# Optimization experiments

Measured on AMD Instinct MI355X. Metric: run time of the kernel, lower is better.

The kernel has to match this reference:

```python
import jax, jax.numpy as jnp
import numpy as np

C = 512
CQK = C // 8  # 64


def setup_inputs() -> dict:
    key = jax.random.key(0)
    ks = jax.random.split(key, 8)
    B, H, W = 16, 32, 32
    x = jax.random.normal(ks[0], (B, C, H, W), dtype=jnp.float32)
    # 1x1 conv weights stored as [out_ch, in_ch] matrices + biases
    sq = 1.0 / np.sqrt(C)
    Wq = jax.random.uniform(ks[1], (CQK, C), jnp.float32, -sq, sq)
    bq = jax.random.uniform(ks[2], (CQK,), jnp.float32, -sq, sq)
    Wk = jax.random.uniform(ks[3], (CQK, C), jnp.float32, -sq, sq)
    bk = jax.random.uniform(ks[4], (CQK,), jnp.float32, -sq, sq)
    Wv = jax.random.uniform(ks[5], (C, C), jnp.float32, -sq, sq)
    bv = jax.random.uniform(ks[6], (C,), jnp.float32, -sq, sq)
    gamma = jax.random.normal(ks[7], (1,), dtype=jnp.float32)
    return {"x": x, "Wq": Wq, "bq": bq, "Wk": Wk, "bk": bk, "Wv": Wv, "bv": bv, "gamma": gamma}


def reference(x, Wq, bq, Wk, bk, Wv, bv, gamma):
    B, Cin, H, W = x.shape
    xf = x.reshape(B, Cin, H * W)  # [B, C, N]
    # 1x1 convs == channel matmuls
    q = jnp.einsum('qc,bcn->bnq', Wq, xf) + bq[None, None, :]   # [B, N, Cqk]
    k = jnp.einsum('qc,bcn->bqn', Wk, xf) + bk[None, :, None]   # [B, Cqk, N]
    v = jnp.einsum('vc,bcn->bvn', Wv, xf) + bv[None, :, None]   # [B, C, N]
    scores = jnp.einsum('bnq,bqm->bnm', q, k)                    # [B, N, N]
    attn = jax.nn.softmax(scores, axis=-1)                       # softmax over keys
    # values @ attn^T : out[b,c,n] = sum_m v[b,c,m] * attn[b,n,m]
    attended = jnp.einsum('bvm,bnm->bvn', v, attn)               # [B, C, N]
    attended = attended.reshape(B, Cin, H, W)
    return gamma[0] * attended + x
```

## Files before the change

kernel.cpp:

```cpp
#include <hip/hip_runtime.h>
#include <stdint.h>

#define BB 16
#define CC 512
#define CQK 64
#define NN 1024

typedef __attribute__((ext_vector_type(8))) short bf16x8;
typedef __attribute__((ext_vector_type(4))) short short4v;
typedef __attribute__((ext_vector_type(8))) unsigned short ushort8;
typedef __attribute__((ext_vector_type(4))) float f32x4;

static __device__ __forceinline__ unsigned short f2bf(float f) {
  uint32_t u = __float_as_uint(f);
  u += 0x7FFFu + ((u >> 16) & 1u);
  return (unsigned short)(u >> 16);
}

static __device__ __forceinline__ void gll16(const unsigned short* g, unsigned short* l) {
  const __attribute__((address_space(1))) unsigned int* gp =
      reinterpret_cast<const __attribute__((address_space(1))) unsigned int*>(
          reinterpret_cast<uintptr_t>(g));
  __attribute__((address_space(3))) unsigned int* lp =
      reinterpret_cast<__attribute__((address_space(3))) unsigned int*>(
          (unsigned int)reinterpret_cast<uintptr_t>(l));
  __builtin_amdgcn_global_load_lds(gp, lp, 16, 0, 0);
}

__global__ __launch_bounds__(256) void k_pack_w(
    const float* __restrict__ Wq, const float* __restrict__ Wk,
    const float* __restrict__ Wv, unsigned short* __restrict__ Wall) {
  int idx = blockIdx.x * 256 + threadIdx.x;
  int e = idx * 4;
  if (e >= 640 * 512) return;
  int o = e >> 9;
  int c = e & 511;
  const float* src;
  if (o < 64)        src = Wq + (size_t)o * 512;
  else if (o < 128)  src = Wk + (size_t)(o - 64) * 512;
  else               src = Wv + (size_t)(o - 128) * 512;
  float4 v = *(const float4*)(src + c);
  short4v pk;
  pk[0] = (short)f2bf(v.x); pk[1] = (short)f2bf(v.y);
  pk[2] = (short)f2bf(v.z); pk[3] = (short)f2bf(v.w);
  *(short4v*)(Wall + e) = pk;
}

__global__ __launch_bounds__(256) void k_transpose_x(
    const float* __restrict__ x, unsigned short* __restrict__ xT) {
  __shared__ float tile[32][33];
  int b = blockIdx.z;
  int c0 = blockIdx.y * 32;
  int n0 = blockIdx.x * 32;
  int t = threadIdx.x;
  int tn = t & 31, tc = t >> 5;
  const float* xp = x + ((size_t)b * CC + c0) * NN + n0;
#pragma unroll
  for (int i = 0; i < 4; i++) {
    int c = tc + i * 8;
    tile[c][tn] = xp[(size_t)c * NN + tn];
  }
  __syncthreads();
  unsigned short* xq = xT + ((size_t)b * NN + n0) * CC + c0;
  int n = t >> 3;
  int cq = (t & 7) * 4;
  short4v pk;
#pragma unroll
  for (int k = 0; k < 4; k++) pk[k] = (short)f2bf(tile[cq + k][n]);
  *(short4v*)(&xq[(size_t)n * CC + cq]) = pk;
}

__global__ __launch_bounds__(256) void k_gemm1(
    const unsigned short* __restrict__ Wall, const unsigned short* __restrict__ xT,
    const float* __restrict__ bq, const float* __restrict__ bk,
    const float* __restrict__ bv,
    unsigned short* __restrict__ qkT, unsigned short* __restrict__ vbuf) {
  __shared__ __align__(16) unsigned short ldsA[2][128 * 32];
  __shared__ __align__(16) unsigned short ldsB[2][128 * 32];
  int bid = blockIdx.x;
  int swz = (bid & 7) * 80 + (bid >> 3);
  int nx = swz & 7;
  int rest = swz >> 3;
  int oy = rest % 5;
  int b = rest / 5;
  int o0 = oy * 128;
  int n0 = nx * 128;
  int t = threadIdx.x;
  int w = t >> 6, l = t & 63;
  int wm = w & 1, wn = w >> 1;
  int lr = l & 15, lq = l >> 4;

  f32x4 acc[4][4];
#pragma unroll
  for (int i = 0; i < 4; i++)
#pragma unroll
    for (int j = 0; j < 4; j++) acc[i][j] = (f32x4){0.f, 0.f, 0.f, 0.f};

  const unsigned short* Ab = Wall + (size_t)o0 * CC;
  const unsigned short* Bb = xT + ((size_t)b * NN + n0) * CC;
  int srow = t >> 2;
  int skq = (t & 3) * 8;
  int ldsw = (t >> 6) * 512;

#pragma unroll
  for (int p = 0; p < 2; p++) {
    int r = p * 64 + srow;
    gll16(&Ab[(size_t)r * CC + skq], &ldsA[0][p * 2048 + ldsw]);
    gll16(&Bb[(size_t)r * CC + skq], &ldsB[0][p * 2048 + ldsw]);
  }
  __syncthreads();

  for (int s = 0; s < 16; ++s) {
    int cur = s & 1;
    if (s + 1 < 16) {
      int kt = (s + 1) * 32;
#pragma unroll
      for (int p = 0; p < 2; p++) {
        int r = p * 64 + srow;
        gll16(&Ab[(size_t)r * CC + kt + skq], &ldsA[cur ^ 1][p * 2048 + ldsw]);
        gll16(&Bb[(size_t)r * CC + kt + skq], &ldsB[cur ^ 1][p * 2048 + ldsw]);
      }
    }
    bf16x8 af[4], bfr[4];
#pragma unroll
    for (int i = 0; i < 4; i++)
      af[i] = *(const bf16x8*)(&ldsA[cur][(wm * 64 + i * 16 + lr) * 32 + lq * 8]);
#pragma unroll
    for (int j = 0; j < 4; j++)
      bfr[j] = *(const bf16x8*)(&ldsB[cur][(wn * 64 + j * 16 + lr) * 32 + lq * 8]);
#pragma unroll
    for (int i = 0; i < 4; i++)
#pragma unroll
      for (int j = 0; j < 4; j++)
        acc[i][j] = __builtin_amdgcn_mfma_f32_16x16x32_bf16(af[i], bfr[j], acc[i][j], 0, 0, 0);
    __syncthreads();
  }

  if (o0 == 0) {
#pragma unroll
    for (int i = 0; i < 4; i++) {
      int ob = wm * 64 + i * 16 + lq * 4;
#pragma unroll
      for (int j = 0; j < 4; j++) {
        int n = n0 + wn * 64 + j * 16 + lr;
        short4v pk;
#pragma unroll
        for (int r = 0; r < 4; r++) {
          int o = ob + r;
          float bias = (o < 64) ? bq[o] : bk[o - 64];
          pk[r] = (short)f2bf(acc[i][j][r] + bias);
        }
        *(short4v*)(&qkT[((size_t)b * NN + n) * 128 + ob]) = pk;
      }
    }
  } else {
#pragma unroll
    for (int i = 0; i < 4; i++) {
#pragma unroll
      for (int r = 0; r < 4; r++) {
        int o = o0 + wm * 64 + i * 16 + lq * 4 + r;
        int c = o - 128;
        float bias = bv[c];
#pragma unroll
        for (int j = 0; j < 4; j++) {
          int n = n0 + wn * 64 + j * 16 + lr;
          vbuf[((size_t)b * CC + c) * NN + n] = f2bf(acc[i][j][r] + bias);
        }
      }
    }
  }
}

#define QT 64
#define MC 64
#define PSTR 72

__global__ __launch_bounds__(256, 2) void k_flash(
    const unsigned short* __restrict__ qkT, const unsigned short* __restrict__ vbuf,
    const float* __restrict__ x, const float* __restrict__ gamma,
    float* __restrict__ out) {
  __shared__ __align__(16) unsigned short P[QT * PSTR];
  __shared__ float red[4 * QT];
  __shared__ float fin[QT];

  int bid = blockIdx.x;
  int swz = (bid & 7) * 64 + (bid >> 3);
  int ntile = swz & 15;
  int chalf = (swz >> 4) & 1;
  int b = swz >> 5;
  int n0 = ntile * QT;
  int t = threadIdx.x;
  int w = t >> 6, l = t & 63;
  int lr = l & 15, lq = l >> 4;
  const unsigned short* qk = qkT + (size_t)b * NN * 128;
  const unsigned short* Vb = vbuf + ((size_t)b * CC + chalf * 256 + w * 64) * NN;

  bf16x8 aq[4][2];
#pragma unroll
  for (int nj = 0; nj < 4; nj++)
#pragma unroll
    for (int ks = 0; ks < 2; ks++)
      aq[nj][ks] = *(const bf16x8*)(&qk[(size_t)(n0 + nj * 16 + lr) * 128 + ks * 32 + lq * 8]);

  f32x4 acc[4][4];
#pragma unroll
  for (int ci = 0; ci < 4; ci++)
#pragma unroll
    for (int nj = 0; nj < 4; nj++) acc[ci][nj] = (f32x4){0.f, 0.f, 0.f, 0.f};
  float sreg[4][4];
#pragma unroll
  for (int nj = 0; nj < 4; nj++)
#pragma unroll
    for (int r = 0; r < 4; r++) sreg[nj][r] = 0.f;

  float ev[4][4];
  {
    int mrow = w * 16 + lr;
    bf16x8 kf0 = *(const bf16x8*)(&qk[(size_t)mrow * 128 + 64 + lq * 8]);
    bf16x8 kf1 = *(const bf16x8*)(&qk[(size_t)mrow * 128 + 96 + lq * 8]);
#pragma unroll
    for (int nj = 0; nj < 4; nj++) {
      f32x4 s = (f32x4){0.f, 0.f, 0.f, 0.f};
      s = __builtin_amdgcn_mfma_f32_16x16x32_bf16(aq[nj][0], kf0, s, 0, 0, 0);
      s = __builtin_amdgcn_mfma_f32_16x16x32_bf16(aq[nj][1], kf1, s, 0, 0, 0);
#pragma unroll
      for (int r = 0; r < 4; r++) {
        float e = __expf(s[r]);
        ev[nj][r] = e;
        sreg[nj][r] += e;
      }
    }
  }

  for (int m0 = 0; m0 < NN; m0 += MC) {
    bf16x8 af0[4];
#pragma unroll
    for (int ci = 0; ci < 4; ci++)
      af0[ci] = *(const bf16x8*)(&Vb[(size_t)(ci * 16 + lr) * NN + m0 + lq * 8]);

    bf16x8 kf0n, kf1n;
    if (m0 + MC < NN) {
      int mrow = m0 + MC + w * 16 + lr;
      kf0n = *(const bf16x8*)(&qk[(size_t)mrow * 128 + 64 + lq * 8]);
      kf1n = *(const bf16x8*)(&qk[(size_t)mrow * 128 + 96 + lq * 8]);
    }

    __syncthreads();
#pragma unroll
    for (int nj = 0; nj < 4; nj++)
#pragma unroll
      for (int r = 0; r < 4; r++)
        P[(nj * 16 + lq * 4 + r) * PSTR + w * 16 + lr] = f2bf(ev[nj][r]);

    if (m0 + MC < NN) {
#pragma unroll
      for (int nj = 0; nj < 4; nj++) {
        f32x4 s = (f32x4){0.f, 0.f, 0.f, 0.f};
        s = __builtin_amdgcn_mfma_f32_16x16x32_bf16(aq[nj][0], kf0n, s, 0, 0, 0);
        s = __builtin_amdgcn_mfma_f32_16x16x32_bf16(aq[nj][1], kf1n, s, 0, 0, 0);
#pragma unroll
        for (int r = 0; r < 4; r++) {
          float e = __expf(s[r]);
          ev[nj][r] = e;
          sreg[nj][r] += e;
        }
      }
    }
    __syncthreads();

    bf16x8 af1[4];
#pragma unroll
    for (int ci = 0; ci < 4; ci++)
      af1[ci] = *(const bf16x8*)(&Vb[(size_t)(ci * 16 + lr) * NN + m0 + 32 + lq * 8]);

#pragma unroll
    for (int nj = 0; nj < 4; nj++) {
      bf16x8 pf = *(const bf16x8*)(&P[(nj * 16 + lr) * PSTR + lq * 8]);
#pragma unroll
      for (int ci = 0; ci < 4; ci++)
        acc[ci][nj] = __builtin_amdgcn_mfma_f32_16x16x32_bf16(af0[ci], pf, acc[ci][nj], 0, 0, 0);
    }
#pragma unroll
    for (int nj = 0; nj < 4; nj++) {
      bf16x8 pf = *(const bf16x8*)(&P[(nj * 16 + lr) * PSTR + 32 + lq * 8]);
#pragma unroll
      for (int ci = 0; ci < 4; ci++)
        acc[ci][nj] = __builtin_amdgcn_mfma_f32_16x16x32_bf16(af1[ci], pf, acc[ci][nj], 0, 0, 0);
    }
  }

#pragma unroll
  for (int nj = 0; nj < 4; nj++)
#pragma unroll
    for (int r = 0; r < 4; r++) {
#pragma unroll
      for (int d = 1; d < 16; d <<= 1) sreg[nj][r] += __shfl_xor(sreg[nj][r], d, 64);
    }
  __syncthreads();
  if (lr == 0) {
#pragma unroll
    for (int nj = 0; nj < 4; nj++)
#pragma unroll
      for (int r = 0; r < 4; r++) red[w * QT + nj * 16 + lq * 4 + r] = sreg[nj][r];
  }
  __syncthreads();
  if (t < QT) {
    float ssum = red[t] + red[QT + t] + red[2 * QT + t] + red[3 * QT + t];
    fin[t] = ssum;
  }
  __syncthreads();

  float invL[4];
#pragma unroll
  for (int nj = 0; nj < 4; nj++) invL[nj] = 1.0f / fin[nj * 16 + lr];
  float g = gamma[0];
#pragma unroll
  for (int ci = 0; ci < 4; ci++) {
#pragma unroll
    for (int r = 0; r < 4; r++) {
      int c = chalf * 256 + w * 64 + ci * 16 + lq * 4 + r;
#pragma unroll
      for (int nj = 0; nj < 4; nj++) {
        size_t idx = ((size_t)b * CC + c) * NN + n0 + nj * 16 + lr;
        out[idx] = g * acc[ci][nj][r] * invL[nj] + x[idx];
      }
    }
  }
}

extern "C" void kernel_launch(void* const* d_in, const int* in_sizes, int n_in,
                              void* d_out, int out_size, void* d_ws, size_t ws_size,
                              hipStream_t stream) {
  (void)in_sizes; (void)n_in; (void)out_size; (void)ws_size;
  const float* x     = (const float*)d_in[0];
  const float* Wq    = (const float*)d_in[1];
  const float* bq    = (const float*)d_in[2];
  const float* Wk    = (const float*)d_in[3];
  const float* bk    = (const float*)d_in[4];
  const float* Wv    = (const float*)d_in[5];
  const float* bv    = (const float*)d_in[6];
  const float* gamma = (const float*)d_in[7];
  float* out = (float*)d_out;

  char* ws = (char*)d_ws;
  unsigned short* Wall = (unsigned short*)(ws);
  unsigned short* xT   = (unsigned short*)(ws + 655360);
  unsigned short* qkT  = (unsigned short*)(ws + 655360 + 16777216);
  unsigned short* vbuf = (unsigned short*)(ws + 655360 + 16777216 + 4194304);

  k_pack_w<<<dim3(320), dim3(256), 0, stream>>>(Wq, Wk, Wv, Wall);
  k_transpose_x<<<dim3(NN / 32, CC / 32, BB), dim3(256), 0, stream>>>(x, xT);
  k_gemm1<<<dim3(640), dim3(256), 0, stream>>>(Wall, xT, bq, bk, bv, qkT, vbuf);
  k_flash<<<dim3(512), dim3(256), 0, stream>>>(qkT, vbuf, x, gamma, out);
}
```

Baseline: 166.6 us.

## Fuse x transpose and bf16 conversion into projection GEMM operand loads

Removes the separate transpose/convert kernel and its 16 MB bf16 intermediate. The projection GEMM now reads fp32 x directly into registers in the MFMA B-operand layout, converting to bf16 on the fly with a one-stage register prefetch. The flash kernel also hoists the second V fragment load ahead of the barrier. In exchange, the global loads of x are scalar strided fp32 reads, each lane hitting 32 different rows. Each x tile is also re-read by five output-row blocks instead of once, and register pressure rises.

```diff
diff --git a/kernel.cpp b/kernel.cpp
--- a/kernel.cpp
+++ b/kernel.cpp
@@ -46,37 +46,12 @@
   *(short4v*)(Wall + e) = pk;
 }
 
-__global__ __launch_bounds__(256) void k_transpose_x(
-    const float* __restrict__ x, unsigned short* __restrict__ xT) {
-  __shared__ float tile[32][33];
-  int b = blockIdx.z;
-  int c0 = blockIdx.y * 32;
-  int n0 = blockIdx.x * 32;
-  int t = threadIdx.x;
-  int tn = t & 31, tc = t >> 5;
-  const float* xp = x + ((size_t)b * CC + c0) * NN + n0;
-#pragma unroll
-  for (int i = 0; i < 4; i++) {
-    int c = tc + i * 8;
-    tile[c][tn] = xp[(size_t)c * NN + tn];
-  }
-  __syncthreads();
-  unsigned short* xq = xT + ((size_t)b * NN + n0) * CC + c0;
-  int n = t >> 3;
-  int cq = (t & 7) * 4;
-  short4v pk;
-#pragma unroll
-  for (int k = 0; k < 4; k++) pk[k] = (short)f2bf(tile[cq + k][n]);
-  *(short4v*)(&xq[(size_t)n * CC + cq]) = pk;
-}
-
 __global__ __launch_bounds__(256) void k_gemm1(
-    const unsigned short* __restrict__ Wall, const unsigned short* __restrict__ xT,
+    const unsigned short* __restrict__ Wall, const float* __restrict__ x,
     const float* __restrict__ bq, const float* __restrict__ bk,
     const float* __restrict__ bv,
     unsigned short* __restrict__ qkT, unsigned short* __restrict__ vbuf) {
   __shared__ __align__(16) unsigned short ldsA[2][128 * 32];
-  __shared__ __align__(16) unsigned short ldsB[2][128 * 32];
   int bid = blockIdx.x;
   int swz = (bid & 7) * 80 + (bid >> 3);
   int nx = swz & 7;
@@ -97,7 +72,7 @@
     for (int j = 0; j < 4; j++) acc[i][j] = (f32x4){0.f, 0.f, 0.f, 0.f};
 
   const unsigned short* Ab = Wall + (size_t)o0 * CC;
-  const unsigned short* Bb = xT + ((size_t)b * NN + n0) * CC;
+  const float* xb2 = x + ((size_t)b * CC) * NN + n0 + wn * 64 + lr;
   int srow = t >> 2;
   int skq = (t & 3) * 8;
   int ldsw = (t >> 6) * 512;
@@ -106,33 +81,56 @@
   for (int p = 0; p < 2; p++) {
     int r = p * 64 + srow;
     gll16(&Ab[(size_t)r * CC + skq], &ldsA[0][p * 2048 + ldsw]);
-    gll16(&Bb[(size_t)r * CC + skq], &ldsB[0][p * 2048 + ldsw]);
+  }
+  float fB[4][8];
+#pragma unroll
+  for (int e = 0; e < 8; e++)
+#pragma unroll
+    for (int j = 0; j < 4; j++)
+      fB[j][e] = xb2[(size_t)(lq * 8 + e) * NN + j * 16];
+  bf16x8 bfr[4];
+#pragma unroll
+  for (int j = 0; j < 4; j++) {
+    bf16x8 v;
+#pragma unroll
+    for (int e = 0; e < 8; e++) v[e] = (short)f2bf(fB[j][e]);
+    bfr[j] = v;
   }
   __syncthreads();
 
   for (int s = 0; s < 16; ++s) {
     int cur = s & 1;
-    if (s + 1 < 16) {
+    if (s < 15) {
       int kt = (s + 1) * 32;
 #pragma unroll
       for (int p = 0; p < 2; p++) {
         int r = p * 64 + srow;
         gll16(&Ab[(size_t)r * CC + kt + skq], &ldsA[cur ^ 1][p * 2048 + ldsw]);
-        gll16(&Bb[(size_t)r * CC + kt + skq], &ldsB[cur ^ 1][p * 2048 + ldsw]);
-      }
-    }
-    bf16x8 af[4], bfr[4];
+      }
+#pragma unroll
+      for (int e = 0; e < 8; e++)
+#pragma unroll
+        for (int j = 0; j < 4; j++)
+          fB[j][e] = xb2[(size_t)(kt + lq * 8 + e) * NN + j * 16];
+    }
+    bf16x8 af[4];
 #pragma unroll
     for (int i = 0; i < 4; i++)
       af[i] = *(const bf16x8*)(&ldsA[cur][(wm * 64 + i * 16 + lr) * 32 + lq * 8]);
 #pragma unroll
-    for (int j = 0; j < 4; j++)
-      bfr[j] = *(const bf16x8*)(&ldsB[cur][(wn * 64 + j * 16 + lr) * 32 + lq * 8]);
-#pragma unroll
     for (int i = 0; i < 4; i++)
 #pragma unroll
       for (int j = 0; j < 4; j++)
         acc[i][j] = __builtin_amdgcn_mfma_f32_16x16x32_bf16(af[i], bfr[j], acc[i][j], 0, 0, 0);
+    if (s < 15) {
+#pragma unroll
+      for (int j = 0; j < 4; j++) {
+        bf16x8 v;
+#pragma unroll
+        for (int e = 0; e < 8; e++) v[e] = (short)f2bf(fB[j][e]);
+        bfr[j] = v;
+      }
+    }
     __syncthreads();
   }
 
@@ -233,10 +231,13 @@
   }
 
   for (int m0 = 0; m0 < NN; m0 += MC) {
-    bf16x8 af0[4];
+    bf16x8 af0[4], af1[4];
 #pragma unroll
     for (int ci = 0; ci < 4; ci++)
       af0[ci] = *(const bf16x8*)(&Vb[(size_t)(ci * 16 + lr) * NN + m0 + lq * 8]);
+#pragma unroll
+    for (int ci = 0; ci < 4; ci++)
+      af1[ci] = *(const bf16x8*)(&Vb[(size_t)(ci * 16 + lr) * NN + m0 + 32 + lq * 8]);
 
     bf16x8 kf0n, kf1n;
     if (m0 + MC < NN) {
@@ -267,11 +268,6 @@
       }
     }
     __syncthreads();
-
-    bf16x8 af1[4];
-#pragma unroll
-    for (int ci = 0; ci < 4; ci++)
-      af1[ci] = *(const bf16x8*)(&Vb[(size_t)(ci * 16 + lr) * NN + m0 + 32 + lq * 8]);
 
 #pragma unroll
     for (int nj = 0; nj < 4; nj++) {
@@ -344,12 +340,10 @@
 
   char* ws = (char*)d_ws;
   unsigned short* Wall = (unsigned short*)(ws);
-  unsigned short* xT   = (unsigned short*)(ws + 655360);
-  unsigned short* qkT  = (unsigned short*)(ws + 655360 + 16777216);
-  unsigned short* vbuf = (unsigned short*)(ws + 655360 + 16777216 + 4194304);
+  unsigned short* qkT  = (unsigned short*)(ws + 655360);
+  unsigned short* vbuf = (unsigned short*)(ws + 655360 + 4194304);
 
   k_pack_w<<<dim3(320), dim3(256), 0, stream>>>(Wq, Wk, Wv, Wall);
-  k_transpose_x<<<dim3(NN / 32, CC / 32, BB), dim3(256), 0, stream>>>(x, xT);
-  k_gemm1<<<dim3(640), dim3(256), 0, stream>>>(Wall, xT, bq, bk, bv, qkT, vbuf);
+  k_gemm1<<<dim3(640), dim3(256), 0, stream>>>(Wall, x, bq, bk, bv, qkT, vbuf);
   k_flash<<<dim3(512), dim3(256), 0, stream>>>(qkT, vbuf, x, gamma, out);
 }
```

After: 178.3 us. +7.0%, slower.

## Fuse all four kernels into one persistent kernel with grid barriers

Applied to the files above, without the earlier changes.

Replaces the four separate launches (weight pack, x transpose, projection GEMM, flash attention) with a single 640-block kernel whose phases are separated by a software grid barrier on a global atomic counter. The aim is to remove launch gaps and tail idle time between the kernels. It also raises launch bounds to 4 blocks per SM and hoists the second V fragment load earlier in the attention loop. The barrier assumes all 640 blocks are co-resident, has a spin timeout that could silently break ordering, and adds atomic spin overhead.

```diff
diff --git a/kernel.cpp b/kernel.cpp
--- a/kernel.cpp
+++ b/kernel.cpp
@@ -5,10 +5,10 @@
 #define CC 512
 #define CQK 64
 #define NN 1024
+#define NBLK 640
 
 typedef __attribute__((ext_vector_type(8))) short bf16x8;
 typedef __attribute__((ext_vector_type(4))) short short4v;
-typedef __attribute__((ext_vector_type(8))) unsigned short ushort8;
 typedef __attribute__((ext_vector_type(4))) float f32x4;
 
 static __device__ __forceinline__ unsigned short f2bf(float f) {
@@ -27,237 +27,226 @@
   __builtin_amdgcn_global_load_lds(gp, lp, 16, 0, 0);
 }
 
-__global__ __launch_bounds__(256) void k_pack_w(
-    const float* __restrict__ Wq, const float* __restrict__ Wk,
-    const float* __restrict__ Wv, unsigned short* __restrict__ Wall) {
-  int idx = blockIdx.x * 256 + threadIdx.x;
-  int e = idx * 4;
-  if (e >= 640 * 512) return;
-  int o = e >> 9;
-  int c = e & 511;
-  const float* src;
-  if (o < 64)        src = Wq + (size_t)o * 512;
-  else if (o < 128)  src = Wk + (size_t)(o - 64) * 512;
-  else               src = Wv + (size_t)(o - 128) * 512;
-  float4 v = *(const float4*)(src + c);
-  short4v pk;
-  pk[0] = (short)f2bf(v.x); pk[1] = (short)f2bf(v.y);
-  pk[2] = (short)f2bf(v.z); pk[3] = (short)f2bf(v.w);
-  *(short4v*)(Wall + e) = pk;
-}
-
-__global__ __launch_bounds__(256) void k_transpose_x(
-    const float* __restrict__ x, unsigned short* __restrict__ xT) {
-  __shared__ float tile[32][33];
-  int b = blockIdx.z;
-  int c0 = blockIdx.y * 32;
-  int n0 = blockIdx.x * 32;
-  int t = threadIdx.x;
-  int tn = t & 31, tc = t >> 5;
-  const float* xp = x + ((size_t)b * CC + c0) * NN + n0;
-#pragma unroll
-  for (int i = 0; i < 4; i++) {
-    int c = tc + i * 8;
-    tile[c][tn] = xp[(size_t)c * NN + tn];
-  }
+__device__ unsigned int g_bar = 0;
+
+static __device__ __forceinline__ void gridbar() {
   __syncthreads();
-  unsigned short* xq = xT + ((size_t)b * NN + n0) * CC + c0;
-  int n = t >> 3;
-  int cq = (t & 7) * 4;
-  short4v pk;
-#pragma unroll
-  for (int k = 0; k < 4; k++) pk[k] = (short)f2bf(tile[cq + k][n]);
-  *(short4v*)(&xq[(size_t)n * CC + cq]) = pk;
-}
-
-__global__ __launch_bounds__(256) void k_gemm1(
-    const unsigned short* __restrict__ Wall, const unsigned short* __restrict__ xT,
-    const float* __restrict__ bq, const float* __restrict__ bk,
-    const float* __restrict__ bv,
-    unsigned short* __restrict__ qkT, unsigned short* __restrict__ vbuf) {
-  __shared__ __align__(16) unsigned short ldsA[2][128 * 32];
-  __shared__ __align__(16) unsigned short ldsB[2][128 * 32];
-  int bid = blockIdx.x;
-  int swz = (bid & 7) * 80 + (bid >> 3);
-  int nx = swz & 7;
-  int rest = swz >> 3;
-  int oy = rest % 5;
-  int b = rest / 5;
-  int o0 = oy * 128;
-  int n0 = nx * 128;
-  int t = threadIdx.x;
-  int w = t >> 6, l = t & 63;
-  int wm = w & 1, wn = w >> 1;
-  int lr = l & 15, lq = l >> 4;
-
-  f32x4 acc[4][4];
-#pragma unroll
-  for (int i = 0; i < 4; i++)
-#pragma unroll
-    for (int j = 0; j < 4; j++) acc[i][j] = (f32x4){0.f, 0.f, 0.f, 0.f};
-
-  const unsigned short* Ab = Wall + (size_t)o0 * CC;
-  const unsigned short* Bb = xT + ((size_t)b * NN + n0) * CC;
-  int srow = t >> 2;
-  int skq = (t & 3) * 8;
-  int ldsw = (t >> 6) * 512;
-
-#pragma unroll
-  for (int p = 0; p < 2; p++) {
-    int r = p * 64 + srow;
-    gll16(&Ab[(size_t)r * CC + skq], &ldsA[0][p * 2048 + ldsw]);
-    gll16(&Bb[(size_t)r * CC + skq], &ldsB[0][p * 2048 + ldsw]);
+  __threadfence();
+  if (threadIdx.x == 0) {
+    unsigned int ticket =
+        __hip_atomic_fetch_add(&g_bar, 1u, __ATOMIC_RELAXED, __HIP_MEMORY_SCOPE_AGENT);
+    unsigned int target = (ticket / NBLK + 1u) * NBLK;
+    unsigned int spins = 0;
+    while (__hip_atomic_load(&g_bar, __ATOMIC_RELAXED, __HIP_MEMORY_SCOPE_AGENT) < target) {
+      __builtin_amdgcn_s_sleep(4);
+      if (++spins > (1u << 20)) break;
+    }
   }
   __syncthreads();
-
-  for (int s = 0; s < 16; ++s) {
-    int cur = s & 1;
-    if (s + 1 < 16) {
-      int kt = (s + 1) * 32;
-#pragma unroll
-      for (int p = 0; p < 2; p++) {
-        int r = p * 64 + srow;
-        gll16(&Ab[(size_t)r * CC + kt + skq], &ldsA[cur ^ 1][p * 2048 + ldsw]);
-        gll16(&Bb[(size_t)r * CC + kt + skq], &ldsB[cur ^ 1][p * 2048 + ldsw]);
-      }
-    }
-    bf16x8 af[4], bfr[4];
-#pragma unroll
-    for (int i = 0; i < 4; i++)
-      af[i] = *(const bf16x8*)(&ldsA[cur][(wm * 64 + i * 16 + lr) * 32 + lq * 8]);
-#pragma unroll
-    for (int j = 0; j < 4; j++)
-      bfr[j] = *(const bf16x8*)(&ldsB[cur][(wn * 64 + j * 16 + lr) * 32 + lq * 8]);
-#pragma unroll
-    for (int i = 0; i < 4; i++)
-#pragma unroll
-      for (int j = 0; j < 4; j++)
-        acc[i][j] = __builtin_amdgcn_mfma_f32_16x16x32_bf16(af[i], bfr[j], acc[i][j], 0, 0, 0);
-    __syncthreads();
-  }
-
-  if (o0 == 0) {
-#pragma unroll
-    for (int i = 0; i < 4; i++) {
-      int ob = wm * 64 + i * 16 + lq * 4;
-#pragma unroll
-      for (int j = 0; j < 4; j++) {
-        int n = n0 + wn * 64 + j * 16 + lr;
-        short4v pk;
-#pragma unroll
-        for (int r = 0; r < 4; r++) {
-          int o = ob + r;
-          float bias = (o < 64) ? bq[o] : bk[o - 64];
-          pk[r] = (short)f2bf(acc[i][j][r] + bias);
-        }
-        *(short4v*)(&qkT[((size_t)b * NN + n) * 128 + ob]) = pk;
-      }
-    }
-  } else {
-#pragma unroll
-    for (int i = 0; i < 4; i++) {
-#pragma unroll
-      for (int r = 0; r < 4; r++) {
-        int o = o0 + wm * 64 + i * 16 + lq * 4 + r;
-        int c = o - 128;
-        float bias = bv[c];
-#pragma unroll
-        for (int j = 0; j < 4; j++) {
-          int n = n0 + wn * 64 + j * 16 + lr;
-          vbuf[((size_t)b * CC + c) * NN + n] = f2bf(acc[i][j][r] + bias);
-        }
-      }
-    }
-  }
+  __threadfence();
 }
 
 #define QT 64
 #define MC 64
 #define PSTR 72
 
-__global__ __launch_bounds__(256, 2) void k_flash(
-    const unsigned short* __restrict__ qkT, const unsigned short* __restrict__ vbuf,
-    const float* __restrict__ x, const float* __restrict__ gamma,
+__global__ __launch_bounds__(256, 4) void k_fused(
+    const float* __restrict__ x,
+    const float* __restrict__ Wq, const float* __restrict__ bq,
+    const float* __restrict__ Wk, const float* __restrict__ bk,
+    const float* __restrict__ Wv, const float* __restrict__ bv,
+    const float* __restrict__ gamma,
+    unsigned short* __restrict__ Wall, unsigned short* __restrict__ xT,
+    unsigned short* __restrict__ qkT, unsigned short* __restrict__ vbuf,
     float* __restrict__ out) {
-  __shared__ __align__(16) unsigned short P[QT * PSTR];
-  __shared__ float red[4 * QT];
-  __shared__ float fin[QT];
+  __shared__ __align__(16) char lds_raw[32768];
 
   int bid = blockIdx.x;
-  int swz = (bid & 7) * 64 + (bid >> 3);
-  int ntile = swz & 15;
-  int chalf = (swz >> 4) & 1;
-  int b = swz >> 5;
-  int n0 = ntile * QT;
   int t = threadIdx.x;
-  int w = t >> 6, l = t & 63;
-  int lr = l & 15, lq = l >> 4;
-  const unsigned short* qk = qkT + (size_t)b * NN * 128;
-  const unsigned short* Vb = vbuf + ((size_t)b * CC + chalf * 256 + w * 64) * NN;
-
-  bf16x8 aq[4][2];
-#pragma unroll
-  for (int nj = 0; nj < 4; nj++)
-#pragma unroll
-    for (int ks = 0; ks < 2; ks++)
-      aq[nj][ks] = *(const bf16x8*)(&qk[(size_t)(n0 + nj * 16 + lr) * 128 + ks * 32 + lq * 8]);
-
-  f32x4 acc[4][4];
-#pragma unroll
-  for (int ci = 0; ci < 4; ci++)
-#pragma unroll
-    for (int nj = 0; nj < 4; nj++) acc[ci][nj] = (f32x4){0.f, 0.f, 0.f, 0.f};
-  float sreg[4][4];
-#pragma unroll
-  for (int nj = 0; nj < 4; nj++)
-#pragma unroll
-    for (int r = 0; r < 4; r++) sreg[nj][r] = 0.f;
-
-  float ev[4][4];
+
+  if (bid < 320) {
+    int e = (bid * 256 + t) * 4;
+    int o = e >> 9;
+    int c = e & 511;
+    const float* src;
+    if (o < 64)        src = Wq + (size_t)o * 512;
+    else if (o < 128)  src = Wk + (size_t)(o - 64) * 512;
+    else               src = Wv + (size_t)(o - 128) * 512;
+    float4 v = *(const float4*)(src + c);
+    short4v pk;
+    pk[0] = (short)f2bf(v.x); pk[1] = (short)f2bf(v.y);
+    pk[2] = (short)f2bf(v.z); pk[3] = (short)f2bf(v.w);
+    *(short4v*)(Wall + e) = pk;
+  }
+
   {
-    int mrow = w * 16 + lr;
-    bf16x8 kf0 = *(const bf16x8*)(&qk[(size_t)mrow * 128 + 64 + lq * 8]);
-    bf16x8 kf1 = *(const bf16x8*)(&qk[(size_t)mrow * 128 + 96 + lq * 8]);
-#pragma unroll
-    for (int nj = 0; nj < 4; nj++) {
-      f32x4 s = (f32x4){0.f, 0.f, 0.f, 0.f};
-      s = __builtin_amdgcn_mfma_f32_16x16x32_bf16(aq[nj][0], kf0, s, 0, 0, 0);
-      s = __builtin_amdgcn_mfma_f32_16x16x32_bf16(aq[nj][1], kf1, s, 0, 0, 0);
-#pragma unroll
-      for (int r = 0; r < 4; r++) {
-        float e = __expf(s[r]);
-        ev[nj][r] = e;
-        sreg[nj][r] += e;
-      }
-    }
-  }
-
-  for (int m0 = 0; m0 < NN; m0 += MC) {
-    bf16x8 af0[4];
+    float (*tile)[33] = (float (*)[33])lds_raw;
+    int tn = t & 31, tc = t >> 5;
+    for (int tau = bid; tau < 8192; tau += NBLK) {
+      int bz = tau >> 9;
+      int by = (tau >> 5) & 15;
+      int bx = tau & 31;
+      int c0 = by * 32, n0 = bx * 32;
+      const float* xp = x + ((size_t)bz * CC + c0) * NN + n0;
+#pragma unroll
+      for (int i = 0; i < 4; i++) {
+        int c = tc + i * 8;
+        tile[c][tn] = xp[(size_t)c * NN + tn];
+      }
+      __syncthreads();
+      unsigned short* xq = xT + ((size_t)bz * NN + n0) * CC + c0;
+      int n = t >> 3;
+      int cq = (t & 7) * 4;
+      short4v pk;
+#pragma unroll
+      for (int k = 0; k < 4; k++) pk[k] = (short)f2bf(tile[cq + k][n]);
+      *(short4v*)(&xq[(size_t)n * CC + cq]) = pk;
+      __syncthreads();
+    }
+  }
+
+  gridbar();
+
+  {
+    unsigned short* ldsA = (unsigned short*)lds_raw;
+    unsigned short* ldsB = ldsA + 8192;
+    int swz = (bid & 7) * 80 + (bid >> 3);
+    int nx = swz & 7;
+    int rest = swz >> 3;
+    int oy = rest % 5;
+    int b = rest / 5;
+    int o0 = oy * 128;
+    int n0 = nx * 128;
+    int w = t >> 6, l = t & 63;
+    int wm = w & 1, wn = w >> 1;
+    int lr = l & 15, lq = l >> 4;
+
+    f32x4 acc[4][4];
+#pragma unroll
+    for (int i = 0; i < 4; i++)
+#pragma unroll
+      for (int j = 0; j < 4; j++) acc[i][j] = (f32x4){0.f, 0.f, 0.f, 0.f};
+
+    const unsigned short* Ab = Wall + (size_t)o0 * CC;
+    const unsigned short* Bb = xT + ((size_t)b * NN + n0) * CC;
+    int srow = t >> 2;
+    int skq = (t & 3) * 8;
+    int ldsw = (t >> 6) * 512;
+
+#pragma unroll
+    for (int p = 0; p < 2; p++) {
+      int r = p * 64 + srow;
+      gll16(&Ab[(size_t)r * CC + skq], &ldsA[p * 2048 + ldsw]);
+      gll16(&Bb[(size_t)r * CC + skq], &ldsB[p * 2048 + ldsw]);
+    }
+    __syncthreads();
+
+    for (int s = 0; s < 16; ++s) {
+      int cur = s & 1;
+      if (s + 1 < 16) {
+        int kt = (s + 1) * 32;
+#pragma unroll
+        for (int p = 0; p < 2; p++) {
+          int r = p * 64 + srow;
+          gll16(&Ab[(size_t)r * CC + kt + skq], &ldsA[(cur ^ 1) * 4096 + p * 2048 + ldsw]);
+          gll16(&Bb[(size_t)r * CC + kt + skq], &ldsB[(cur ^ 1) * 4096 + p * 2048 + ldsw]);
+        }
+      }
+      bf16x8 af[4], bfr[4];
+#pragma unroll
+      for (int i = 0; i < 4; i++)
+        af[i] = *(const bf16x8*)(&ldsA[cur * 4096 + (wm * 64 + i * 16 + lr) * 32 + lq * 8]);
+#pragma unroll
+      for (int j = 0; j < 4; j++)
+        bfr[j] = *(const bf16x8*)(&ldsB[cur * 4096 + (wn * 64 + j * 16 + lr) * 32 + lq * 8]);
+#pragma unroll
+      for (int i = 0; i < 4; i++)
+#pragma unroll
+        for (int j = 0; j < 4; j++)
+          acc[i][j] = __builtin_amdgcn_mfma_f32_16x16x32_bf16(af[i], bfr[j], acc[i][j], 0, 0, 0);
+      __syncthreads();
+    }
+
+    if (o0 == 0) {
+#pragma unroll
+      for (int i = 0; i < 4; i++) {
+        int ob = wm * 64 + i * 16 + lq * 4;
+#pragma unroll
+        for (int j = 0; j < 4; j++) {
+          int n = n0 + wn * 64 + j * 16 + lr;
+          short4v pk;
+#pragma unroll
+          for (int r = 0; r < 4; r++) {
+            int o = ob + r;
+            float bias = (o < 64) ? bq[o] : bk[o - 64];
+            pk[r] = (short)f2bf(acc[i][j][r] + bias);
+          }
+          *(short4v*)(&qkT[((size_t)b * NN + n) * 128 + ob]) = pk;
+        }
+      }
+    } else {
+#pragma unroll
+      for (int i = 0; i < 4; i++) {
+#pragma unroll
+        for (int r = 0; r < 4; r++) {
+          int o = o0 + wm * 64 + i * 16 + lq * 4 + r;
+          int c = o - 128;
+          float bias = bv[c];
+#pragma unroll
+          for (int j = 0; j < 4; j++) {
+            int n = n0 + wn * 64 + j * 16 + lr;
+            vbuf[((size_t)b * CC + c) * NN + n] = f2bf(acc[i][j][r] + bias);
+          }
+        }
+      }
+    }
+  }
+
+  gridbar();
+
+  if (bid < 512) {
+    unsigned short* P = (unsigned short*)lds_raw;
+    float* red = (float*)(lds_raw + 9216);
+    float* fin = (float*)(lds_raw + 9216 + 1024);
+
+    int swz = (bid & 7) * 64 + (bid >> 3);
+    int ntile = swz & 15;
+    int chalf = (swz >> 4) & 1;
+    int b = swz >> 5;
+    int n0 = ntile * QT;
+    int w = t >> 6, l = t & 63;
+    int lr = l & 15, lq = l >> 4;
+    const unsigned short* qk = qkT + (size_t)b * NN * 128;
+    const unsigned short* Vb = vbuf + ((size_t)b * CC + chalf * 256 + w * 64) * NN;
+
+    bf16x8 aq[4][2];
+#pragma unroll
+    for (int nj = 0; nj < 4; nj++)
+#pragma unroll
+      for (int ks = 0; ks < 2; ks++)
+        aq[nj][ks] = *(const bf16x8*)(&qk[(size_t)(n0 + nj * 16 + lr) * 128 + ks * 32 + lq * 8]);
+
+    f32x4 acc[4][4];
 #pragma unroll
     for (int ci = 0; ci < 4; ci++)
-      af0[ci] = *(const bf16x8*)(&Vb[(size_t)(ci * 16 + lr) * NN + m0 + lq * 8]);
-
-    bf16x8 kf0n, kf1n;
-    if (m0 + MC < NN) {
-      int mrow = m0 + MC + w * 16 + lr;
-      kf0n = *(const bf16x8*)(&qk[(size_t)mrow * 128 + 64 + lq * 8]);
-      kf1n = *(const bf16x8*)(&qk[(size_t)mrow * 128 + 96 + lq * 8]);
-    }
-
-    __syncthreads();
+#pragma unroll
+      for (int nj = 0; nj < 4; nj++) acc[ci][nj] = (f32x4){0.f, 0.f, 0.f, 0.f};
+    float sreg[4][4];
 #pragma unroll
     for (int nj = 0; nj < 4; nj++)
 #pragma unroll
-      for (int r = 0; r < 4; r++)
-        P[(nj * 16 + lq * 4 + r) * PSTR + w * 16 + lr] = f2bf(ev[nj][r]);
-
-    if (m0 + MC < NN) {
+      for (int r = 0; r < 4; r++) sreg[nj][r] = 0.f;
+
+    float ev[4][4];
+    {
+      int mrow = w * 16 + lr;
+      bf16x8 kf0 = *(const bf16x8*)(&qk[(size_t)mrow * 128 + 64 + lq * 8]);
+      bf16x8 kf1 = *(const bf16x8*)(&qk[(size_t)mrow * 128 + 96 + lq * 8]);
 #pragma unroll
       for (int nj = 0; nj < 4; nj++) {
         f32x4 s = (f32x4){0.f, 0.f, 0.f, 0.f};
-        s = __builtin_amdgcn_mfma_f32_16x16x32_bf16(aq[nj][0], kf0n, s, 0, 0, 0);
-        s = __builtin_amdgcn_mfma_f32_16x16x32_bf16(aq[nj][1], kf1n, s, 0, 0, 0);
+        s = __builtin_amdgcn_mfma_f32_16x16x32_bf16(aq[nj][0], kf0, s, 0, 0, 0);
+        s = __builtin_amdgcn_mfma_f32_16x16x32_bf16(aq[nj][1], kf1, s, 0, 0, 0);
 #pragma unroll
         for (int r = 0; r < 4; r++) {
           float e = __expf(s[r]);
@@ -266,63 +255,97 @@
         }
       }
     }
+
+    for (int m0 = 0; m0 < NN; m0 += MC) {
+      bf16x8 af0[4], af1[4];
+#pragma unroll
+      for (int ci = 0; ci < 4; ci++)
+        af0[ci] = *(const bf16x8*)(&Vb[(size_t)(ci * 16 + lr) * NN + m0 + lq * 8]);
+#pragma unroll
+      for (int ci = 0; ci < 4; ci++)
+        af1[ci] = *(const bf16x8*)(&Vb[(size_t)(ci * 16 + lr) * NN + m0 + 32 + lq * 8]);
+
+      bf16x8 kf0n, kf1n;
+      if (m0 + MC < NN) {
+        int mrow = m0 + MC + w * 16 + lr;
+        kf0n = *(const bf16x8*)(&qk[(size_t)mrow * 128 + 64 + lq * 8]);
+        kf1n = *(const bf16x8*)(&qk[(size_t)mrow * 128 + 96 + lq * 8]);
+      }
+
+      __syncthreads();
+#pragma unroll
+      for (int nj = 0; nj < 4; nj++)
+#pragma unroll
+        for (int r = 0; r < 4; r++)
+          P[(nj * 16 + lq * 4 + r) * PSTR + w * 16 + lr] = f2bf(ev[nj][r]);
+
+      if (m0 + MC < NN) {
+#pragma unroll
+        for (int nj = 0; nj < 4; nj++) {
+          f32x4 s = (f32x4){0.f, 0.f, 0.f, 0.f};
+          s = __builtin_amdgcn_mfma_f32_16x16x32_bf16(aq[nj][0], kf0n, s, 0, 0, 0);
+          s = __builtin_amdgcn_mfma_f32_16x16x32_bf16(aq[nj][1], kf1n, s, 0, 0, 0);
+#pragma unroll
+          for (int r = 0; r < 4; r++) {
+            float e = __expf(s[r]);
+            ev[nj][r] = e;
+            sreg[nj][r] += e;
+          }
+        }
+      }
+      __syncthreads();
+
+#pragma unroll
+      for (int nj = 0; nj < 4; nj++) {
+        bf16x8 pf = *(const bf16x8*)(&P[(nj * 16 + lr) * PSTR + lq * 8]);
+#pragma unroll
+        for (int ci = 0; ci < 4; ci++)
+          acc[ci][nj] = __builtin_amdgcn_mfma_f32_16x16x32_bf16(af0[ci], pf, acc[ci][nj], 0, 0, 0);
+      }
+#pragma unroll
+      for (int nj = 0; nj < 4; nj++) {
+        bf16x8 pf = *(const bf16x8*)(&P[(nj * 16 + lr) * PSTR + 32 + lq * 8]);
+#pragma unroll
+        for (int ci = 0; ci < 4; ci++)
+          acc[ci][nj] = __builtin_amdgcn_mfma_f32_16x16x32_bf16(af1[ci], pf, acc[ci][nj], 0, 0, 0);
+      }
+    }
+
+#pragma unroll
+    for (int nj = 0; nj < 4; nj++)
+#pragma unroll
+      for (int r = 0; r < 4; r++) {
+#pragma unroll
+        for (int d = 1; d < 16; d <<= 1) sreg[nj][r] += __shfl_xor(sreg[nj][r], d, 64);
+      }
     __syncthreads();
-
-    bf16x8 af1[4];
-#pragma unroll
-    for (int ci = 0; ci < 4; ci++)
-      af1[ci] = *(const bf16x8*)(&Vb[(size_t)(ci * 16 + lr) * NN + m0 + 32 + lq * 8]);
-
-#pragma unroll
-    for (int nj = 0; nj < 4; nj++) {
-      bf16x8 pf = *(const bf16x8*)(&P[(nj * 16 + lr) * PSTR + lq * 8]);
-#pragma unroll
-      for (int ci = 0; ci < 4; ci++)
-        acc[ci][nj] = __builtin_amdgcn_mfma_f32_16x16x32_bf16(af0[ci], pf, acc[ci][nj], 0, 0, 0);
-    }
-#pragma unroll
-    for (int nj = 0; nj < 4; nj++) {
-      bf16x8 pf = *(const bf16x8*)(&P[(nj * 16 + lr) * PSTR + 32 + lq * 8]);
-#pragma unroll
-      for (int ci = 0; ci < 4; ci++)
-        acc[ci][nj] = __builtin_amdgcn_mfma_f32_16x16x32_bf16(af1[ci], pf, acc[ci][nj], 0, 0, 0);
-    }
-  }
-
-#pragma unroll
-  for (int nj = 0; nj < 4; nj++)
-#pragma unroll
-    for (int r = 0; r < 4; r++) {
-#pragma unroll
-      for (int d = 1; d < 16; d <<= 1) sreg[nj][r] += __shfl_xor(sreg[nj][r], d, 64);
-    }
-  __syncthreads();
-  if (lr == 0) {
-#pragma unroll
-    for (int nj = 0; nj < 4; nj++)
-#pragma unroll
-      for (int r = 0; r < 4; r++) red[w * QT + nj * 16 + lq * 4 + r] = sreg[nj][r];
-  }
-  __syncthreads();
-  if (t < QT) {
-    float ssum = red[t] + red[QT + t] + red[2 * QT + t] + red[3 * QT + t];
-    fin[t] = ssum;
-  }
-  __syncthreads();
-
-  float invL[4];
-#pragma unroll
-  for (int nj = 0; nj < 4; nj++) invL[nj] = 1.0f / fin[nj * 16 + lr];
-  float g = gamma[0];
-#pragma unroll
-  for (int ci = 0; ci < 4; ci++) {
-#pragma unroll
-    for (int r = 0; r < 4; r++) {
-      int c = chalf * 256 + w * 64 + ci * 16 + lq * 4 + r;
-#pragma unroll
-      for (int nj = 0; nj < 4; nj++) {
-        size_t idx = ((size_t)b * CC + c) * NN + n0 + nj * 16 + lr;
-        out[idx] = g * acc[ci][nj][r] * invL[nj] + x[idx];
+    if (lr == 0) {
+#pragma unroll
+      for (int nj = 0; nj < 4; nj++)
+#pragma unroll
+        for (int r = 0; r < 4; r++) red[w * QT + nj * 16 + lq * 4 + r] = sreg[nj][r];
+    }
+    __syncthreads();
+    if (t < QT) {
+      float ssum = red[t] + red[QT + t] + red[2 * QT + t] + red[3 * QT + t];
+      fin[t] = ssum;
+    }
+    __syncthreads();
+
+    float invL[4];
+#pragma unroll
+    for (int nj = 0; nj < 4; nj++) invL[nj] = 1.0f / fin[nj * 16 + lr];
+    float g = gamma[0];
+#pragma unroll
+    for (int ci = 0; ci < 4; ci++) {
+#pragma unroll
+      for (int r = 0; r < 4; r++) {
+        int c = chalf * 256 + w * 64 + ci * 16 + lq * 4 + r;
+#pragma unroll
+        for (int nj = 0; nj < 4; nj++) {
+          size_t idx = ((size_t)b * CC + c) * NN + n0 + nj * 16 + lr;
+          out[idx] = g * acc[ci][nj][r] * invL[nj] + x[idx];
+        }
       }
     }
   }
@@ -348,8 +371,6 @@
   unsigned short* qkT  = (unsigned short*)(ws + 655360 + 16777216);
   unsigned short* vbuf = (unsigned short*)(ws + 655360 + 16777216 + 4194304);
 
-  k_pack_w<<<dim3(320), dim3(256), 0, stream>>>(Wq, Wk, Wv, Wall);
-  k_transpose_x<<<dim3(NN / 32, CC / 32, BB), dim3(256), 0, stream>>>(x, xT);
-  k_gemm1<<<dim3(640), dim3(256), 0, stream>>>(Wall, xT, bq, bk, bv, qkT, vbuf);
-  k_flash<<<dim3(512), dim3(256), 0, stream>>>(qkT, vbuf, x, gamma, out);
-}
+  k_fused<<<dim3(NBLK), dim3(256), 0, stream>>>(
+      x, Wq, bq, Wk, bk, Wv, bv, gamma, Wall, xT, qkT, vbuf, out);
+}
```

Result: slower. 541.2 us (+224.8%).

## Fuse weight packing into transpose kernel and deepen V/K prefetch in flash loop

Applied to the files above, without the earlier changes.

Folds the weight bf16 packing into the x-transpose kernel, so the first 320 blocks also convert weights and one launch is removed. In the attention kernel, V fragments for the next chunk and K fragments two chunks ahead are prefetched into registers, so global-load latency is overlapped across loop iterations instead of stalling inside each one. The cost is higher register pressure, which under launch_bounds(256,2) may cause spills or lower occupancy.

```diff
diff --git a/kernel.cpp b/kernel.cpp
--- a/kernel.cpp
+++ b/kernel.cpp
@@ -8,7 +8,6 @@
 
 typedef __attribute__((ext_vector_type(8))) short bf16x8;
 typedef __attribute__((ext_vector_type(4))) short short4v;
-typedef __attribute__((ext_vector_type(8))) unsigned short ushort8;
 typedef __attribute__((ext_vector_type(4))) float f32x4;
 
 static __device__ __forceinline__ unsigned short f2bf(float f) {
@@ -27,32 +26,32 @@
   __builtin_amdgcn_global_load_lds(gp, lp, 16, 0, 0);
 }
 
-__global__ __launch_bounds__(256) void k_pack_w(
+__global__ __launch_bounds__(256) void k_prep(
+    const float* __restrict__ x, unsigned short* __restrict__ xT,
     const float* __restrict__ Wq, const float* __restrict__ Wk,
     const float* __restrict__ Wv, unsigned short* __restrict__ Wall) {
-  int idx = blockIdx.x * 256 + threadIdx.x;
-  int e = idx * 4;
-  if (e >= 640 * 512) return;
-  int o = e >> 9;
-  int c = e & 511;
-  const float* src;
-  if (o < 64)        src = Wq + (size_t)o * 512;
-  else if (o < 128)  src = Wk + (size_t)(o - 64) * 512;
-  else               src = Wv + (size_t)(o - 128) * 512;
-  float4 v = *(const float4*)(src + c);
-  short4v pk;
-  pk[0] = (short)f2bf(v.x); pk[1] = (short)f2bf(v.y);
-  pk[2] = (short)f2bf(v.z); pk[3] = (short)f2bf(v.w);
-  *(short4v*)(Wall + e) = pk;
-}
-
-__global__ __launch_bounds__(256) void k_transpose_x(
-    const float* __restrict__ x, unsigned short* __restrict__ xT) {
   __shared__ float tile[32][33];
   int b = blockIdx.z;
   int c0 = blockIdx.y * 32;
   int n0 = blockIdx.x * 32;
   int t = threadIdx.x;
+
+  int flat = ((int)blockIdx.z * gridDim.y + blockIdx.y) * gridDim.x + blockIdx.x;
+  if (flat < 320) {
+    int e = (flat * 256 + t) * 4;
+    int o = e >> 9;
+    int c = e & 511;
+    const float* src;
+    if (o < 64)        src = Wq + (size_t)o * 512;
+    else if (o < 128)  src = Wk + (size_t)(o - 64) * 512;
+    else               src = Wv + (size_t)(o - 128) * 512;
+    float4 v = *(const float4*)(src + c);
+    short4v pk;
+    pk[0] = (short)f2bf(v.x); pk[1] = (short)f2bf(v.y);
+    pk[2] = (short)f2bf(v.z); pk[3] = (short)f2bf(v.w);
+    *(short4v*)(Wall + e) = pk;
+  }
+
   int tn = t & 31, tc = t >> 5;
   const float* xp = x + ((size_t)b * CC + c0) * NN + n0;
 #pragma unroll
@@ -192,6 +191,7 @@
   int t = threadIdx.x;
   int w = t >> 6, l = t & 63;
   int lr = l & 15, lq = l >> 4;
+  int lq8 = lq * 8;
   const unsigned short* qk = qkT + (size_t)b * NN * 128;
   const unsigned short* Vb = vbuf + ((size_t)b * CC + chalf * 256 + w * 64) * NN;
 
@@ -200,7 +200,7 @@
   for (int nj = 0; nj < 4; nj++)
 #pragma unroll
     for (int ks = 0; ks < 2; ks++)
-      aq[nj][ks] = *(const bf16x8*)(&qk[(size_t)(n0 + nj * 16 + lr) * 128 + ks * 32 + lq * 8]);
+      aq[nj][ks] = *(const bf16x8*)(&qk[(size_t)(n0 + nj * 16 + lr) * 128 + ks * 32 + lq8]);
 
   f32x4 acc[4][4];
 #pragma unroll
@@ -213,11 +213,21 @@
 #pragma unroll
     for (int r = 0; r < 4; r++) sreg[nj][r] = 0.f;
 
+  bf16x8 vA[4];
+#pragma unroll
+  for (int ci = 0; ci < 4; ci++)
+    vA[ci] = *(const bf16x8*)(&Vb[(size_t)(ci * 16 + lr) * NN + lq8]);
+  bf16x8 kf0c, kf1c;
+  {
+    int mrow = MC + w * 16 + lr;
+    kf0c = *(const bf16x8*)(&qk[(size_t)mrow * 128 + 64 + lq8]);
+    kf1c = *(const bf16x8*)(&qk[(size_t)mrow * 128 + 96 + lq8]);
+  }
   float ev[4][4];
   {
     int mrow = w * 16 + lr;
-    bf16x8 kf0 = *(const bf16x8*)(&qk[(size_t)mrow * 128 + 64 + lq * 8]);
-    bf16x8 kf1 = *(const bf16x8*)(&qk[(size_t)mrow * 128 + 96 + lq * 8]);
+    bf16x8 kf0 = *(const bf16x8*)(&qk[(size_t)mrow * 128 + 64 + lq8]);
+    bf16x8 kf1 = *(const bf16x8*)(&qk[(size_t)mrow * 128 + 96 + lq8]);
 #pragma unroll
     for (int nj = 0; nj < 4; nj++) {
       f32x4 s = (f32x4){0.f, 0.f, 0.f, 0.f};
@@ -233,16 +243,22 @@
   }
 
   for (int m0 = 0; m0 < NN; m0 += MC) {
-    bf16x8 af0[4];
+    bool hn = (m0 + MC < NN);
+    bf16x8 vB[4];
 #pragma unroll
     for (int ci = 0; ci < 4; ci++)
-      af0[ci] = *(const bf16x8*)(&Vb[(size_t)(ci * 16 + lr) * NN + m0 + lq * 8]);
-
+      vB[ci] = *(const bf16x8*)(&Vb[(size_t)(ci * 16 + lr) * NN + m0 + 32 + lq8]);
+    bf16x8 vAn[4];
+    if (hn) {
+#pragma unroll
+      for (int ci = 0; ci < 4; ci++)
+        vAn[ci] = *(const bf16x8*)(&Vb[(size_t)(ci * 16 + lr) * NN + m0 + MC + lq8]);
+    }
     bf16x8 kf0n, kf1n;
-    if (m0 + MC < NN) {
-      int mrow = m0 + MC + w * 16 + lr;
-      kf0n = *(const bf16x8*)(&qk[(size_t)mrow * 128 + 64 + lq * 8]);
-      kf1n = *(const bf16x8*)(&qk[(size_t)mrow * 128 + 96 + lq * 8]);
+    if (m0 + 2 * MC < NN) {
+      int mrow = m0 + 2 * MC + w * 16 + lr;
+      kf0n = *(const bf16x8*)(&qk[(size_t)mrow * 128 + 64 + lq8]);
+      kf1n = *(const bf16x8*)(&qk[(size_t)mrow * 128 + 96 + lq8]);
     }
 
     __syncthreads();
@@ -252,12 +268,12 @@
       for (int r = 0; r < 4; r++)
         P[(nj * 16 + lq * 4 + r) * PSTR + w * 16 + lr] = f2bf(ev[nj][r]);
 
-    if (m0 + MC < NN) {
+    if (hn) {
 #pragma unroll
       for (int nj = 0; nj < 4; nj++) {
         f32x4 s = (f32x4){0.f, 0.f, 0.f, 0.f};
-        s = __builtin_amdgcn_mfma_f32_16x16x32_bf16(aq[nj][0], kf0n, s, 0, 0, 0);
-        s = __builtin_amdgcn_mfma_f32_16x16x32_bf16(aq[nj][1], kf1n, s, 0, 0, 0);
+        s = __builtin_amdgcn_mfma_f32_16x16x32_bf16(aq[nj][0], kf0c, s, 0, 0, 0);
+        s = __builtin_amdgcn_mfma_f32_16x16x32_bf16(aq[nj][1], kf1c, s, 0, 0, 0);
 #pragma unroll
         for (int r = 0; r < 4; r++) {
           float e = __expf(s[r]);
@@ -268,24 +284,26 @@
     }
     __syncthreads();
 
-    bf16x8 af1[4];
-#pragma unroll
-    for (int ci = 0; ci < 4; ci++)
-      af1[ci] = *(const bf16x8*)(&Vb[(size_t)(ci * 16 + lr) * NN + m0 + 32 + lq * 8]);
-
 #pragma unroll
     for (int nj = 0; nj < 4; nj++) {
-      bf16x8 pf = *(const bf16x8*)(&P[(nj * 16 + lr) * PSTR + lq * 8]);
+      bf16x8 pf = *(const bf16x8*)(&P[(nj * 16 + lr) * PSTR + lq8]);
 #pragma unroll
       for (int ci = 0; ci < 4; ci++)
-        acc[ci][nj] = __builtin_amdgcn_mfma_f32_16x16x32_bf16(af0[ci], pf, acc[ci][nj], 0, 0, 0);
+        acc[ci][nj] = __builtin_amdgcn_mfma_f32_16x16x32_bf16(vA[ci], pf, acc[ci][nj], 0, 0, 0);
     }
 #pragma unroll
     for (int nj = 0; nj < 4; nj++) {
-      bf16x8 pf = *(const bf16x8*)(&P[(nj * 16 + lr) * PSTR + 32 + lq * 8]);
+      bf16x8 pf = *(const bf16x8*)(&P[(nj * 16 + lr) * PSTR + 32 + lq8]);
 #pragma unroll
       for (int ci = 0; ci < 4; ci++)
-        acc[ci][nj] = __builtin_amdgcn_mfma_f32_16x16x32_bf16(af1[ci], pf, acc[ci][nj], 0, 0, 0);
+        acc[ci][nj] = __builtin_amdgcn_mfma_f32_16x16x32_bf16(vB[ci], pf, acc[ci][nj], 0, 0, 0);
+    }
+
+    if (hn) {
+#pragma unroll
+      for (int ci = 0; ci < 4; ci++) vA[ci] = vAn[ci];
+      kf0c = kf0n;
+      kf1c = kf1n;
     }
   }
 
@@ -348,8 +366,7 @@
   unsigned short* qkT  = (unsigned short*)(ws + 655360 + 16777216);
   unsigned short* vbuf = (unsigned short*)(ws + 655360 + 16777216 + 4194304);
 
-  k_pack_w<<<dim3(320), dim3(256), 0, stream>>>(Wq, Wk, Wv, Wall);
-  k_transpose_x<<<dim3(NN / 32, CC / 32, BB), dim3(256), 0, stream>>>(x, xT);
+  k_prep<<<dim3(NN / 32, CC / 32, BB), dim3(256), 0, stream>>>(x, xT, Wq, Wk, Wv, Wall);
   k_gemm1<<<dim3(640), dim3(256), 0, stream>>>(Wall, xT, bq, bk, bv, qkT, vbuf);
   k_flash<<<dim3(512), dim3(256), 0, stream>>>(qkT, vbuf, x, gamma, out);
 }
```

New measurement: 165.5 us. No clear change (-0.7%).
